# Performance work log

Hardware: AMD Instinct MI355X
Metric: run time of the kernel (lower is better)

The kernel has to match this reference:

```python
import jax, jax.numpy as jnp
import numpy as np


def setup_inputs() -> dict:
    key = jax.random.key(0)
    ks = jax.random.split(key, 4)
    B, S, H = 1, 2048, 2048
    E, I = 32, 768
    scale_h = 1.0 / np.sqrt(H)
    scale_i = 1.0 / np.sqrt(I)
    return {
        "hidden_states": jax.random.normal(ks[0], (B, S, H), dtype=jnp.float32),
        "gate_w": jax.random.normal(ks[1], (E, H), dtype=jnp.float32) * scale_h,
        "gate_up_proj": jax.random.normal(ks[2], (E, H, 2 * I), dtype=jnp.float32) * scale_h,
        "down_proj": jax.random.normal(ks[3], (E, I, H), dtype=jnp.float32) * scale_i,
    }


TOP_K = 4


def reference(hidden_states, gate_w, gate_up_proj, down_proj):
    B, S, H = hidden_states.shape
    x = hidden_states.reshape(-1, H)                      # [T, H]
    T = x.shape[0]

    # Router: softmax -> top-k -> renormalize -> scatter back to dense [T, E]
    router_logits = x @ gate_w.T                          # [T, E]
    probs = jax.nn.softmax(router_logits.astype(jnp.float32), axis=-1)
    top_w, top_idx = jax.lax.top_k(probs, TOP_K)          # [T, K]
    top_w = top_w / jnp.sum(top_w, axis=-1, keepdims=True)
    top_w = top_w.astype(x.dtype)
    router_weights = jnp.zeros_like(router_logits).at[
        jnp.arange(T)[:, None], top_idx
    ].set(top_w)                                          # [T, E]

    # Experts (eval path): every expert processes every token, then weight & sum.
    gate_up = jnp.einsum("th,ehi->eti", x, gate_up_proj)  # [E, T, 2I]
    gate, up = jnp.split(gate_up, 2, axis=-1)
    h = up * jax.nn.silu(gate)                            # [E, T, I]
    expert_out = jnp.einsum("eti,eih->eth", h, down_proj)  # [E, T, H]
    out = jnp.einsum("eth,te->th", expert_out, router_weights)  # [T, H]

    return out.reshape(B, S, H), router_logits
```

## Files before the change

### kernel.cpp

```cpp
#include <hip/hip_runtime.h>
#include <hip/hip_bf16.h>

#define T_TOK 2048
#define H_DIM 2048
#define E_NUM 32
#define I_DIM 768
#define TOPK  4
#define S4    (T_TOK * TOPK)

typedef __attribute__((ext_vector_type(8))) short bf16x8;
typedef __attribute__((ext_vector_type(4))) float f32x4;

__device__ __forceinline__ unsigned pk2(float a, float b) {
    __hip_bfloat16 ha = __float2bfloat16(a);
    __hip_bfloat16 hb = __float2bfloat16(b);
    unsigned short ua = *(unsigned short*)&ha;
    unsigned short ub = *(unsigned short*)&hb;
    return (unsigned)ua | ((unsigned)ub << 16);
}

#define MFMA16(a, b, c) __builtin_amdgcn_mfma_f32_16x16x32_bf16(a, b, c, 0, 0, 0)

__global__ __launch_bounds__(64) void router_kernel(
    const float* __restrict__ x, const float* __restrict__ gate_w,
    float* __restrict__ logits_out, int* __restrict__ cnt,
    int* __restrict__ tok_list, float* __restrict__ tok_w,
    int* __restrict__ tok_slots)
{
    const int t = blockIdx.x;
    const int lane = threadIdx.x;
    __shared__ float xs[H_DIM];
    const float4* __restrict__ xv = (const float4*)(x + (size_t)t * H_DIM);
    float4* xsv = (float4*)xs;
#pragma unroll
    for (int i = 0; i < H_DIM / 4 / 64; ++i) xsv[lane + i * 64] = xv[lane + i * 64];
    __syncthreads();

    const int e = lane & 31;
    const int half = lane >> 5;
    const float4* __restrict__ wv = (const float4*)(gate_w + (size_t)e * H_DIM) + half * (H_DIM / 8);
    const float4* __restrict__ xh = ((const float4*)xs) + half * (H_DIM / 8);
    float acc = 0.f;
#pragma unroll 4
    for (int i = 0; i < H_DIM / 8; ++i) {
        float4 w4 = wv[i], x4 = xh[i];
        acc += w4.x * x4.x + w4.y * x4.y + w4.z * x4.z + w4.w * x4.w;
    }
    acc += __shfl_xor(acc, 32, 64);
    if (lane < 32) logits_out[(size_t)t * E_NUM + e] = acc;

    float v = acc;
    float topv[TOPK]; int topi[TOPK];
#pragma unroll
    for (int r = 0; r < TOPK; ++r) {
        float bv = v; int bi = e;
#pragma unroll
        for (int off = 16; off >= 1; off >>= 1) {
            float ov = __shfl_xor(bv, off, 32);
            int   oi = __shfl_xor(bi, off, 32);
            if (ov > bv || (ov == bv && oi < bi)) { bv = ov; bi = oi; }
        }
        topv[r] = bv; topi[r] = bi;
        if (e == bi) v = -1e30f;
    }
    if (lane == 0) {
        float w[TOPK]; float s = 0.f;
#pragma unroll
        for (int r = 0; r < TOPK; ++r) { w[r] = expf(topv[r] - topv[0]); s += w[r]; }
        float inv = 1.f / s;
#pragma unroll
        for (int r = 0; r < TOPK; ++r) {
            int pos = atomicAdd(&cnt[topi[r]], 1);
            tok_list[topi[r] * T_TOK + pos] = t;
            tok_w  [topi[r] * T_TOK + pos] = w[r] * inv;
            tok_slots[t * TOPK + r] = (topi[r] << 12) | pos;
        }
    }
}

__global__ void scan_kernel(const int* __restrict__ cnt, int* __restrict__ slot_base)
{
    if (threadIdx.x == 0) {
        int s = 0;
        for (int e = 0; e < E_NUM; ++e) { slot_base[e] = s; s += cnt[e]; }
        slot_base[E_NUM] = s;
    }
}

__global__ __launch_bounds__(256) void gather_kernel(
    const float* __restrict__ x, const int* __restrict__ cnt,
    const int* __restrict__ slot_base, const int* __restrict__ tok_list,
    unsigned short* __restrict__ xg_t)
{
    const int e = blockIdx.x;
    const int count = cnt[e];
    const int m0 = blockIdx.y * 8;
    if (m0 >= count) return;
    const int s8   = threadIdx.x >> 5;
    const int kc31 = threadIdx.x & 31;
    const int m = m0 + s8;
    if (m >= count) return;
    const int tok  = tok_list[e * T_TOK + m];
    const int slot = slot_base[e] + m;
    const float* __restrict__ src = x + (size_t)tok * H_DIM;
#pragma unroll
    for (int kcq = 0; kcq < 8; ++kcq) {
        const int kc = kcq * 32 + kc31;
        float4 a = *(const float4*)(src + kc * 8);
        float4 b = *(const float4*)(src + kc * 8 + 4);
        uint4 o;
        o.x = pk2(a.x, a.y); o.y = pk2(a.z, a.w);
        o.z = pk2(b.x, b.y); o.w = pk2(b.z, b.w);
        *(uint4*)(xg_t + ((size_t)kc * S4 + slot) * 8) = o;
    }
}

#define GU_NC (H_DIM / 128)
__global__ __launch_bounds__(512, 4) void gateup_mfma(
    const unsigned short* __restrict__ xg_t, const float* __restrict__ gup_w,
    const int* __restrict__ cnt, const int* __restrict__ slot_base,
    const float* __restrict__ tok_w, unsigned short* __restrict__ h_t)
{
    const int e  = blockIdx.x;
    const int nt = blockIdx.y;
    const int mt = blockIdx.z;
    const int count = cnt[e];
    if (mt * 256 >= count) return;
    const int tid  = threadIdx.x;
    const int lane = tid & 63;
    const int w    = tid >> 6;
    const int base = slot_base[e];
    const int l16  = lane & 15, lg = lane >> 4;

    __shared__ unsigned short Bls[2][2][16 * 32 * 8];
    __shared__ float wls[256];

    if (tid < 256) {
        int m = mt * 256 + tid; if (m >= count) m = count - 1;
        wls[tid] = tok_w[e * T_TOK + m];
    }

    int m0 = mt * 256 + w * 32 + l16;      if (m0 >= count) m0 = count - 1;
    int m1 = mt * 256 + w * 32 + 16 + l16; if (m1 >= count) m1 = count - 1;
    const unsigned short* a0b = xg_t + (size_t)(base + m0) * 8;
    const unsigned short* a1b = xg_t + (size_t)(base + m1) * 8;

    const int bhalf = tid >> 8;
    const int sub   = (tid >> 7) & 1;
    const int t7    = tid & 127;
    const int kb    = (t7 >> 3) * 2;
    const int n4    = (t7 & 7) * 4;
    const int k8    = kb & 7;
    const int kbh   = kb >> 3;
    const float* __restrict__ bbase =
        gup_w + ((size_t)e * H_DIM + kb) * (2 * I_DIM) + (size_t)bhalf * I_DIM + nt * 32 + n4;

    float4 sv0[2], sv1[2];

#define GU_LOAD(C) do { _Pragma("unroll") for (int q2 = 0; q2 < 2; ++q2) { \
        const int q = sub + q2 * 2; \
        const float* s_ = bbase + (size_t)((C) * 128 + q * 32) * (2 * I_DIM); \
        sv0[q2] = *(const float4*)s_; \
        sv1[q2] = *(const float4*)(s_ + 2 * I_DIM); } } while (0)
#define GU_WRITE(BUF) do { _Pragma("unroll") for (int q2 = 0; q2 < 2; ++q2) { \
        const int q = sub + q2 * 2; \
        unsigned short* bw_ = &Bls[BUF][bhalf][((q * 4 + kbh) * 32) * 8]; \
        float p0[4] = {sv0[q2].x, sv0[q2].y, sv0[q2].z, sv0[q2].w}; \
        float p1[4] = {sv1[q2].x, sv1[q2].y, sv1[q2].z, sv1[q2].w}; \
        _Pragma("unroll") for (int j = 0; j < 4; ++j) \
            *(unsigned*)&bw_[(n4 + j) * 8 + k8] = pk2(p0[j], p1[j]); } } while (0)

    f32x4 accg[2][2], accu[2][2];
#pragma unroll
    for (int i = 0; i < 2; ++i)
#pragma unroll
        for (int f = 0; f < 2; ++f) { accg[i][f] = {0.f,0.f,0.f,0.f}; accu[i][f] = {0.f,0.f,0.f,0.f}; }

    GU_LOAD(0);
    GU_WRITE(0);

    for (int c = 0; c < GU_NC; ++c) {
        const int buf = c & 1;
        __syncthreads();
        if (c + 1 < GU_NC) GU_LOAD(c + 1);
#pragma unroll
        for (int s = 0; s < 4; ++s) {
            const size_t aoff = (size_t)(c * 16 + s * 4 + lg) * (S4 * 8);
            bf16x8 a0 = *(const bf16x8*)(a0b + aoff);
            bf16x8 a1 = *(const bf16x8*)(a1b + aoff);
            const unsigned short* bg_ = &Bls[buf][0][((s * 4 + lg) * 32 + l16) * 8];
            const unsigned short* bu_ = &Bls[buf][1][((s * 4 + lg) * 32 + l16) * 8];
            bf16x8 g0 = *(const bf16x8*)(bg_);
            bf16x8 g1 = *(const bf16x8*)(bg_ + 128);
            bf16x8 u0 = *(const bf16x8*)(bu_);
            bf16x8 u1 = *(const bf16x8*)(bu_ + 128);
            accg[0][0] = MFMA16(a0, g0, accg[0][0]);
            accg[0][1] = MFMA16(a0, g1, accg[0][1]);
            accu[0][0] = MFMA16(a0, u0, accu[0][0]);
            accu[0][1] = MFMA16(a0, u1, accu[0][1]);
            accg[1][0] = MFMA16(a1, g0, accg[1][0]);
            accg[1][1] = MFMA16(a1, g1, accg[1][1]);
            accu[1][0] = MFMA16(a1, u0, accu[1][0]);
            accu[1][1] = MFMA16(a1, u1, accu[1][1]);
        }
        if (c + 1 < GU_NC) GU_WRITE((c + 1) & 1);
    }
#undef GU_LOAD
#undef GU_WRITE

#pragma unroll
    for (int i = 0; i < 2; ++i) {
        const int mloc = w * 32 + i * 16 + lg * 4;
#pragma unroll
        for (int r = 0; r < 4; ++r) {
            const int mrow = mt * 256 + mloc + r;
            if (mrow < count) {
                const float wgt = wls[mloc + r];
                const size_t slot = (size_t)(base + mrow);
#pragma unroll
                for (int f = 0; f < 2; ++f) {
                    const int col = nt * 32 + f * 16 + l16;
                    float g = accg[i][f][r], u = accu[i][f][r];
                    float sv = g / (1.f + expf(-g));
                    __hip_bfloat16 hb = __float2bfloat16(wgt * u * sv);
                    h_t[((size_t)(col >> 3) * S4 + slot) * 8 + (col & 7)] = *(unsigned short*)&hb;
                }
            }
        }
    }
}

#define DN_NC (I_DIM / 128)
__global__ __launch_bounds__(512, 4) void down_mfma(
    const unsigned short* __restrict__ h_t, const float* __restrict__ down_w,
    const int* __restrict__ cnt, const int* __restrict__ slot_base,
    float* __restrict__ ods)
{
    const int e  = blockIdx.x;
    const int nt = blockIdx.y;
    const int mt = blockIdx.z;
    const int count = cnt[e];
    if (mt * 256 >= count) return;
    const int tid  = threadIdx.x;
    const int lane = tid & 63;
    const int w    = tid >> 6;
    const int base = slot_base[e];
    const int l16  = lane & 15, lg = lane >> 4;

    __shared__ unsigned short Bls[2][16 * 64 * 8];

    int m0 = mt * 256 + w * 32 + l16;      if (m0 >= count) m0 = count - 1;
    int m1 = mt * 256 + w * 32 + 16 + l16; if (m1 >= count) m1 = count - 1;
    const unsigned short* a0b = h_t + (size_t)(base + m0) * 8;
    const unsigned short* a1b = h_t + (size_t)(base + m1) * 8;

    const int sub = tid >> 8;
    const int t8  = tid & 255;
    const int kb  = (t8 >> 4) * 2;
    const int n4  = (t8 & 15) * 4;
    const int k8  = kb & 7;
    const int kbh = kb >> 3;
    const float* __restrict__ bbase =
        down_w + ((size_t)e * I_DIM + kb) * H_DIM + nt * 64 + n4;

    float4 sv0[2], sv1[2];

#define DN_LOAD(C) do { _Pragma("unroll") for (int q2 = 0; q2 < 2; ++q2) { \
        const int q = sub + q2 * 2; \
        const float* s_ = bbase + (size_t)((C) * 128 + q * 32) * H_DIM; \
        sv0[q2] = *(const float4*)s_; \
        sv1[q2] = *(const float4*)(s_ + H_DIM); } } while (0)
#define DN_WRITE(BUF) do { _Pragma("unroll") for (int q2 = 0; q2 < 2; ++q2) { \
        const int q = sub + q2 * 2; \
        unsigned short* bw_ = &Bls[BUF][((q * 4 + kbh) * 64) * 8]; \
        float p0[4] = {sv0[q2].x, sv0[q2].y, sv0[q2].z, sv0[q2].w}; \
        float p1[4] = {sv1[q2].x, sv1[q2].y, sv1[q2].z, sv1[q2].w}; \
        _Pragma("unroll") for (int j = 0; j < 4; ++j) \
            *(unsigned*)&bw_[(n4 + j) * 8 + k8] = pk2(p0[j], p1[j]); } } while (0)

    f32x4 acc[2][4];
#pragma unroll
    for (int i = 0; i < 2; ++i)
#pragma unroll
        for (int f = 0; f < 4; ++f) acc[i][f] = {0.f,0.f,0.f,0.f};

    DN_LOAD(0);
    DN_WRITE(0);

    for (int c = 0; c < DN_NC; ++c) {
        const int buf = c & 1;
        __syncthreads();
        if (c + 1 < DN_NC) DN_LOAD(c + 1);
#pragma unroll
        for (int s = 0; s < 4; ++s) {
            const size_t aoff = (size_t)(c * 16 + s * 4 + lg) * (S4 * 8);
            bf16x8 a0 = *(const bf16x8*)(a0b + aoff);
            bf16x8 a1 = *(const bf16x8*)(a1b + aoff);
            const unsigned short* bf_ = &Bls[buf][((s * 4 + lg) * 64 + l16) * 8];
            bf16x8 b0 = *(const bf16x8*)(bf_);
            bf16x8 b1 = *(const bf16x8*)(bf_ + 128);
            bf16x8 b2 = *(const bf16x8*)(bf_ + 256);
            bf16x8 b3 = *(const bf16x8*)(bf_ + 384);
            acc[0][0] = MFMA16(a0, b0, acc[0][0]);
            acc[0][1] = MFMA16(a0, b1, acc[0][1]);
            acc[0][2] = MFMA16(a0, b2, acc[0][2]);
            acc[0][3] = MFMA16(a0, b3, acc[0][3]);
            acc[1][0] = MFMA16(a1, b0, acc[1][0]);
            acc[1][1] = MFMA16(a1, b1, acc[1][1]);
            acc[1][2] = MFMA16(a1, b2, acc[1][2]);
            acc[1][3] = MFMA16(a1, b3, acc[1][3]);
        }
        if (c + 1 < DN_NC) DN_WRITE((c + 1) & 1);
    }
#undef DN_LOAD
#undef DN_WRITE

#pragma unroll
    for (int i = 0; i < 2; ++i) {
        const int mloc = w * 32 + i * 16 + lg * 4;
#pragma unroll
        for (int r = 0; r < 4; ++r) {
            const int mrow = mt * 256 + mloc + r;
            if (mrow < count) {
                float* orow = ods + (size_t)(base + mrow) * H_DIM + nt * 64;
#pragma unroll
                for (int f = 0; f < 4; ++f)
                    orow[f * 16 + l16] = acc[i][f][r];
            }
        }
    }
}

__global__ __launch_bounds__(256) void combine_kernel(
    const float* __restrict__ ods, const int* __restrict__ tok_slots,
    const int* __restrict__ slot_base, float* __restrict__ out)
{
    const int t = blockIdx.x;
    const int c0 = threadIdx.x * 8;
    const float* rows[TOPK];
#pragma unroll
    for (int r = 0; r < TOPK; ++r) {
        const int pk = tok_slots[t * TOPK + r];
        const int e = pk >> 12, pos = pk & 4095;
        rows[r] = ods + (size_t)(slot_base[e] + pos) * H_DIM + c0;
    }
    float4 a0 = {0.f,0.f,0.f,0.f}, a1 = {0.f,0.f,0.f,0.f};
#pragma unroll
    for (int r = 0; r < TOPK; ++r) {
        float4 v0 = *(const float4*)(rows[r]);
        float4 v1 = *(const float4*)(rows[r] + 4);
        a0.x += v0.x; a0.y += v0.y; a0.z += v0.z; a0.w += v0.w;
        a1.x += v1.x; a1.y += v1.y; a1.z += v1.z; a1.w += v1.w;
    }
    float* o = out + (size_t)t * H_DIM + c0;
    *(float4*)o = a0;
    *(float4*)(o + 4) = a1;
}

extern "C" void kernel_launch(void* const* d_in, const int* in_sizes, int n_in,
                              void* d_out, int out_size, void* d_ws, size_t ws_size,
                              hipStream_t stream) {
    const float* x      = (const float*)d_in[0];
    const float* gate_w = (const float*)d_in[1];
    const float* gup_w  = (const float*)d_in[2];
    const float* down_w = (const float*)d_in[3];
    float* out    = (float*)d_out;

    char* wsp = (char*)d_ws;
    int*   cnt       = (int*)(wsp);
    int*   slot_base = (int*)(wsp + 256);
    int*   tok_list  = (int*)(wsp + 4096);
    float* tok_w     = (float*)(wsp + 4096 + (size_t)E_NUM * T_TOK * 4);
    int*   tok_slots = (int*)(wsp + (768u << 10));
    unsigned short* xg_t = (unsigned short*)(wsp + (1u << 20));
    unsigned short* h_t  = (unsigned short*)(wsp + (1u << 20) + (size_t)S4 * H_DIM * 2);
    float* ods = (float*)(wsp + (1u << 20) + (size_t)S4 * H_DIM * 2 + (size_t)S4 * I_DIM * 2);

    hipMemsetAsync(cnt, 0, 256, stream);

    router_kernel<<<T_TOK, 64, 0, stream>>>(x, gate_w, out + (size_t)T_TOK * H_DIM,
                                            cnt, tok_list, tok_w, tok_slots);
    scan_kernel<<<1, 64, 0, stream>>>(cnt, slot_base);
    gather_kernel<<<dim3(E_NUM, 256), 256, 0, stream>>>(x, cnt, slot_base, tok_list, xg_t);
    gateup_mfma<<<dim3(E_NUM, 24, 8), 512, 0, stream>>>(
        xg_t, gup_w, cnt, slot_base, tok_w, h_t);
    down_mfma<<<dim3(E_NUM, 32, 8), 512, 0, stream>>>(
        h_t, down_w, cnt, slot_base, ods);
    combine_kernel<<<T_TOK, 256, 0, stream>>>(ods, tok_slots, slot_base, out);
}
```

Baseline: 458.7 us.

## Pre-pack expert weights to bf16 tile images and stage via global_load_lds

Result: slower. 514.5 us (+12.2%).

```diff
diff --git a/kernel.cpp b/kernel.cpp
--- a/kernel.cpp
+++ b/kernel.cpp
@@ -7,6 +7,8 @@
 #define I_DIM 768
 #define TOPK  4
 #define S4    (T_TOK * TOPK)
+#define GU_IMG 8192
+#define DN_IMG 8192
 
 typedef __attribute__((ext_vector_type(8))) short bf16x8;
 typedef __attribute__((ext_vector_type(4))) float f32x4;
@@ -17,6 +19,12 @@
     unsigned short ua = *(unsigned short*)&ha;
     unsigned short ub = *(unsigned short*)&hb;
     return (unsigned)ua | ((unsigned)ub << 16);
+}
+
+__device__ __forceinline__ void gld16(const void* g, void* l) {
+    __builtin_amdgcn_global_load_lds(
+        (const __attribute__((address_space(1))) void*)g,
+        (__attribute__((address_space(3))) void*)l, 16, 0, 0);
 }
 
 #define MFMA16(a, b, c) __builtin_amdgcn_mfma_f32_16x16x32_bf16(a, b, c, 0, 0, 0)
@@ -84,6 +92,70 @@
         int s = 0;
         for (int e = 0; e < E_NUM; ++e) { slot_base[e] = s; s += cnt[e]; }
         slot_base[E_NUM] = s;
+    }
+}
+
+__global__ __launch_bounds__(256) void pack_gu(
+    const float* __restrict__ gup_w, unsigned short* __restrict__ pgu)
+{
+    const int e  = blockIdx.x;
+    const int kg = blockIdx.y;
+    const int c  = kg >> 4, kk = kg & 15;
+    __shared__ unsigned short ls[8][1538];
+    const float* __restrict__ src = gup_w + ((size_t)e * H_DIM + kg * 8) * (2 * I_DIM);
+#pragma unroll
+    for (int r = 0; r < 8; ++r) {
+        const float4* s4 = (const float4*)(src + (size_t)r * (2 * I_DIM));
+        for (int i = threadIdx.x; i < (2 * I_DIM) / 4; i += 256) {
+            float4 v = s4[i];
+            *(unsigned*)&ls[r][i * 4]     = pk2(v.x, v.y);
+            *(unsigned*)&ls[r][i * 4 + 2] = pk2(v.z, v.w);
+        }
+    }
+    __syncthreads();
+    for (int g = threadIdx.x; g < 2 * I_DIM; g += 256) {
+        const int half = g >= I_DIM;
+        const int cg = g - half * I_DIM;
+        const int nt = cg >> 5, n = cg & 31;
+        uint4 o;
+        o.x = (unsigned)ls[0][g] | ((unsigned)ls[1][g] << 16);
+        o.y = (unsigned)ls[2][g] | ((unsigned)ls[3][g] << 16);
+        o.z = (unsigned)ls[4][g] | ((unsigned)ls[5][g] << 16);
+        o.w = (unsigned)ls[6][g] | ((unsigned)ls[7][g] << 16);
+        unsigned short* dst = pgu + ((size_t)(e * 24 + nt) * 16 + c) * GU_IMG
+                            + ((half * 16 + kk) * 32 + n) * 8;
+        *(uint4*)dst = o;
+    }
+}
+
+__global__ __launch_bounds__(256) void pack_dn(
+    const float* __restrict__ down_w, unsigned short* __restrict__ pdn)
+{
+    const int e  = blockIdx.x;
+    const int kg = blockIdx.y;
+    const int c  = kg >> 4, kk = kg & 15;
+    __shared__ unsigned short ls[8][2050];
+    const float* __restrict__ src = down_w + ((size_t)e * I_DIM + kg * 8) * H_DIM;
+#pragma unroll
+    for (int r = 0; r < 8; ++r) {
+        const float4* s4 = (const float4*)(src + (size_t)r * H_DIM);
+        for (int i = threadIdx.x; i < H_DIM / 4; i += 256) {
+            float4 v = s4[i];
+            *(unsigned*)&ls[r][i * 4]     = pk2(v.x, v.y);
+            *(unsigned*)&ls[r][i * 4 + 2] = pk2(v.z, v.w);
+        }
+    }
+    __syncthreads();
+    for (int g = threadIdx.x; g < H_DIM; g += 256) {
+        const int nt = g >> 6, n = g & 63;
+        uint4 o;
+        o.x = (unsigned)ls[0][g] | ((unsigned)ls[1][g] << 16);
+        o.y = (unsigned)ls[2][g] | ((unsigned)ls[3][g] << 16);
+        o.z = (unsigned)ls[4][g] | ((unsigned)ls[5][g] << 16);
+        o.w = (unsigned)ls[6][g] | ((unsigned)ls[7][g] << 16);
+        unsigned short* dst = pdn + ((size_t)(e * 32 + nt) * 6 + c) * DN_IMG
+                            + (kk * 64 + n) * 8;
+        *(uint4*)dst = o;
     }
 }
 
@@ -117,7 +189,7 @@
 
 #define GU_NC (H_DIM / 128)
 __global__ __launch_bounds__(512, 4) void gateup_mfma(
-    const unsigned short* __restrict__ xg_t, const float* __restrict__ gup_w,
+    const unsigned short* __restrict__ xg_t, const unsigned short* __restrict__ pgu,
     const int* __restrict__ cnt, const int* __restrict__ slot_base,
     const float* __restrict__ tok_w, unsigned short* __restrict__ h_t)
 {
@@ -132,7 +204,7 @@
     const int base = slot_base[e];
     const int l16  = lane & 15, lg = lane >> 4;
 
-    __shared__ unsigned short Bls[2][2][16 * 32 * 8];
+    __shared__ unsigned short Bls[2][GU_IMG];
     __shared__ float wls[256];
 
     if (tid < 256) {
@@ -145,30 +217,12 @@
     const unsigned short* a0b = xg_t + (size_t)(base + m0) * 8;
     const unsigned short* a1b = xg_t + (size_t)(base + m1) * 8;
 
-    const int bhalf = tid >> 8;
-    const int sub   = (tid >> 7) & 1;
-    const int t7    = tid & 127;
-    const int kb    = (t7 >> 3) * 2;
-    const int n4    = (t7 & 7) * 4;
-    const int k8    = kb & 7;
-    const int kbh   = kb >> 3;
-    const float* __restrict__ bbase =
-        gup_w + ((size_t)e * H_DIM + kb) * (2 * I_DIM) + (size_t)bhalf * I_DIM + nt * 32 + n4;
-
-    float4 sv0[2], sv1[2];
-
-#define GU_LOAD(C) do { _Pragma("unroll") for (int q2 = 0; q2 < 2; ++q2) { \
-        const int q = sub + q2 * 2; \
-        const float* s_ = bbase + (size_t)((C) * 128 + q * 32) * (2 * I_DIM); \
-        sv0[q2] = *(const float4*)s_; \
-        sv1[q2] = *(const float4*)(s_ + 2 * I_DIM); } } while (0)
-#define GU_WRITE(BUF) do { _Pragma("unroll") for (int q2 = 0; q2 < 2; ++q2) { \
-        const int q = sub + q2 * 2; \
-        unsigned short* bw_ = &Bls[BUF][bhalf][((q * 4 + kbh) * 32) * 8]; \
-        float p0[4] = {sv0[q2].x, sv0[q2].y, sv0[q2].z, sv0[q2].w}; \
-        float p1[4] = {sv1[q2].x, sv1[q2].y, sv1[q2].z, sv1[q2].w}; \
-        _Pragma("unroll") for (int j = 0; j < 4; ++j) \
-            *(unsigned*)&bw_[(n4 + j) * 8 + k8] = pk2(p0[j], p1[j]); } } while (0)
+    const unsigned short* __restrict__ bimg = pgu + ((size_t)(e * 24 + nt) * 16) * GU_IMG;
+
+#define GU_STAGE(C, BUF) do { \
+    const unsigned short* s_ = bimg + (size_t)(C) * GU_IMG + w * 1024 + lane * 8; \
+    gld16(s_,       &Bls[BUF][w * 1024]); \
+    gld16(s_ + 512, &Bls[BUF][w * 1024 + 512]); } while (0)
 
     f32x4 accg[2][2], accu[2][2];
 #pragma unroll
@@ -176,20 +230,19 @@
 #pragma unroll
         for (int f = 0; f < 2; ++f) { accg[i][f] = {0.f,0.f,0.f,0.f}; accu[i][f] = {0.f,0.f,0.f,0.f}; }
 
-    GU_LOAD(0);
-    GU_WRITE(0);
+    GU_STAGE(0, 0);
 
     for (int c = 0; c < GU_NC; ++c) {
         const int buf = c & 1;
         __syncthreads();
-        if (c + 1 < GU_NC) GU_LOAD(c + 1);
+        if (c + 1 < GU_NC) GU_STAGE(c + 1, buf ^ 1);
 #pragma unroll
         for (int s = 0; s < 4; ++s) {
             const size_t aoff = (size_t)(c * 16 + s * 4 + lg) * (S4 * 8);
             bf16x8 a0 = *(const bf16x8*)(a0b + aoff);
             bf16x8 a1 = *(const bf16x8*)(a1b + aoff);
-            const unsigned short* bg_ = &Bls[buf][0][((s * 4 + lg) * 32 + l16) * 8];
-            const unsigned short* bu_ = &Bls[buf][1][((s * 4 + lg) * 32 + l16) * 8];
+            const unsigned short* bg_ = &Bls[buf][((s * 4 + lg) * 32 + l16) * 8];
+            const unsigned short* bu_ = bg_ + 4096;
             bf16x8 g0 = *(const bf16x8*)(bg_);
             bf16x8 g1 = *(const bf16x8*)(bg_ + 128);
             bf16x8 u0 = *(const bf16x8*)(bu_);
@@ -203,10 +256,8 @@
             accu[1][0] = MFMA16(a1, u0, accu[1][0]);
             accu[1][1] = MFMA16(a1, u1, accu[1][1]);
         }
-        if (c + 1 < GU_NC) GU_WRITE((c + 1) & 1);
-    }
-#undef GU_LOAD
-#undef GU_WRITE
+    }
+#undef GU_STAGE
 
 #pragma unroll
     for (int i = 0; i < 2; ++i) {
@@ -232,7 +283,7 @@
 
 #define DN_NC (I_DIM / 128)
 __global__ __launch_bounds__(512, 4) void down_mfma(
-    const unsigned short* __restrict__ h_t, const float* __restrict__ down_w,
+    const unsigned short* __restrict__ h_t, const unsigned short* __restrict__ pdn,
     const int* __restrict__ cnt, const int* __restrict__ slot_base,
     float* __restrict__ ods)
 {
@@ -247,36 +298,19 @@
     const int base = slot_base[e];
     const int l16  = lane & 15, lg = lane >> 4;
 
-    __shared__ unsigned short Bls[2][16 * 64 * 8];
+    __shared__ unsigned short Bls[2][DN_IMG];
 
     int m0 = mt * 256 + w * 32 + l16;      if (m0 >= count) m0 = count - 1;
     int m1 = mt * 256 + w * 32 + 16 + l16; if (m1 >= count) m1 = count - 1;
     const unsigned short* a0b = h_t + (size_t)(base + m0) * 8;
     const unsigned short* a1b = h_t + (size_t)(base + m1) * 8;
 
-    const int sub = tid >> 8;
-    const int t8  = tid & 255;
-    const int kb  = (t8 >> 4) * 2;
-    const int n4  = (t8 & 15) * 4;
-    const int k8  = kb & 7;
-    const int kbh = kb >> 3;
-    const float* __restrict__ bbase =
-        down_w + ((size_t)e * I_DIM + kb) * H_DIM + nt * 64 + n4;
-
-    float4 sv0[2], sv1[2];
-
-#define DN_LOAD(C) do { _Pragma("unroll") for (int q2 = 0; q2 < 2; ++q2) { \
-        const int q = sub + q2 * 2; \
-        const float* s_ = bbase + (size_t)((C) * 128 + q * 32) * H_DIM; \
-        sv0[q2] = *(const float4*)s_; \
-        sv1[q2] = *(const float4*)(s_ + H_DIM); } } while (0)
-#define DN_WRITE(BUF) do { _Pragma("unroll") for (int q2 = 0; q2 < 2; ++q2) { \
-        const int q = sub + q2 * 2; \
-        unsigned short* bw_ = &Bls[BUF][((q * 4 + kbh) * 64) * 8]; \
-        float p0[4] = {sv0[q2].x, sv0[q2].y, sv0[q2].z, sv0[q2].w}; \
-        float p1[4] = {sv1[q2].x, sv1[q2].y, sv1[q2].z, sv1[q2].w}; \
-        _Pragma("unroll") for (int j = 0; j < 4; ++j) \
-            *(unsigned*)&bw_[(n4 + j) * 8 + k8] = pk2(p0[j], p1[j]); } } while (0)
+    const unsigned short* __restrict__ bimg = pdn + ((size_t)(e * 32 + nt) * 6) * DN_IMG;
+
+#define DN_STAGE(C, BUF) do { \
+    const unsigned short* s_ = bimg + (size_t)(C) * DN_IMG + w * 1024 + lane * 8; \
+    gld16(s_,       &Bls[BUF][w * 1024]); \
+    gld16(s_ + 512, &Bls[BUF][w * 1024 + 512]); } while (0)
 
     f32x4 acc[2][4];
 #pragma unroll
@@ -284,13 +318,12 @@
 #pragma unroll
         for (int f = 0; f < 4; ++f) acc[i][f] = {0.f,0.f,0.f,0.f};
 
-    DN_LOAD(0);
-    DN_WRITE(0);
+    DN_STAGE(0, 0);
 
     for (int c = 0; c < DN_NC; ++c) {
         const int buf = c & 1;
         __syncthreads();
-        if (c + 1 < DN_NC) DN_LOAD(c + 1);
+        if (c + 1 < DN_NC) DN_STAGE(c + 1, buf ^ 1);
 #pragma unroll
         for (int s = 0; s < 4; ++s) {
             const size_t aoff = (size_t)(c * 16 + s * 4 + lg) * (S4 * 8);
@@ -310,10 +343,8 @@
             acc[1][2] = MFMA16(a1, b2, acc[1][2]);
             acc[1][3] = MFMA16(a1, b3, acc[1][3]);
         }
-        if (c + 1 < DN_NC) DN_WRITE((c + 1) & 1);
-    }
-#undef DN_LOAD
-#undef DN_WRITE
+    }
+#undef DN_STAGE
 
 #pragma unroll
     for (int i = 0; i < 2; ++i) {
@@ -372,19 +403,25 @@
     int*   tok_list  = (int*)(wsp + 4096);
     float* tok_w     = (float*)(wsp + 4096 + (size_t)E_NUM * T_TOK * 4);
     int*   tok_slots = (int*)(wsp + (768u << 10));
-    unsigned short* xg_t = (unsigned short*)(wsp + (1u << 20));
-    unsigned short* h_t  = (unsigned short*)(wsp + (1u << 20) + (size_t)S4 * H_DIM * 2);
-    float* ods = (float*)(wsp + (1u << 20) + (size_t)S4 * H_DIM * 2 + (size_t)S4 * I_DIM * 2);
+
+    size_t off = (size_t)1 << 20;
+    unsigned short* xg_t = (unsigned short*)(wsp + off); off += (size_t)S4 * H_DIM * 2;
+    unsigned short* h_t  = (unsigned short*)(wsp + off); off += (size_t)S4 * I_DIM * 2;
+    float*          ods  = (float*)(wsp + off);          off += (size_t)S4 * H_DIM * 4;
+    unsigned short* pgu  = (unsigned short*)(wsp + off); off += (size_t)E_NUM * 24 * 16 * GU_IMG * 2;
+    unsigned short* pdn  = (unsigned short*)(wsp + off); off += (size_t)E_NUM * 32 * 6 * DN_IMG * 2;
 
     hipMemsetAsync(cnt, 0, 256, stream);
 
     router_kernel<<<T_TOK, 64, 0, stream>>>(x, gate_w, out + (size_t)T_TOK * H_DIM,
                                             cnt, tok_list, tok_w, tok_slots);
     scan_kernel<<<1, 64, 0, stream>>>(cnt, slot_base);
+    pack_gu<<<dim3(E_NUM, 256), 256, 0, stream>>>(gup_w, pgu);
+    pack_dn<<<dim3(E_NUM, 96), 256, 0, stream>>>(down_w, pdn);
     gather_kernel<<<dim3(E_NUM, 256), 256, 0, stream>>>(x, cnt, slot_base, tok_list, xg_t);
     gateup_mfma<<<dim3(E_NUM, 24, 8), 512, 0, stream>>>(
-        xg_t, gup_w, cnt, slot_base, tok_w, h_t);
+        xg_t, pgu, cnt, slot_base, tok_w, h_t);
     down_mfma<<<dim3(E_NUM, 32, 8), 512, 0, stream>>>(
-        h_t, down_w, cnt, slot_base, ods);
+        h_t, pdn, cnt, slot_base, ods);
     combine_kernel<<<T_TOK, 256, 0, stream>>>(ods, tok_slots, slot_base, out);
 }
```

## Split-K both expert GEMMs with atomic accumulation and separate SiLU pass

Applied to the files above, without the earlier changes.

Result: slower. 666.4 us (+45.3%).

```diff
diff --git a/kernel.cpp b/kernel.cpp
--- a/kernel.cpp
+++ b/kernel.cpp
@@ -20,6 +20,13 @@
 }
 
 #define MFMA16(a, b, c) __builtin_amdgcn_mfma_f32_16x16x32_bf16(a, b, c, 0, 0, 0)
+
+__global__ __launch_bounds__(256) void zero_kernel(uint4* __restrict__ p, long n16)
+{
+    long i = (long)blockIdx.x * 256 + threadIdx.x;
+    long stride = (long)gridDim.x * 256;
+    for (; i < n16; i += stride) p[i] = (uint4){0u, 0u, 0u, 0u};
+}
 
 __global__ __launch_bounds__(64) void router_kernel(
     const float* __restrict__ x, const float* __restrict__ gate_w,
@@ -90,7 +97,8 @@
 __global__ __launch_bounds__(256) void gather_kernel(
     const float* __restrict__ x, const int* __restrict__ cnt,
     const int* __restrict__ slot_base, const int* __restrict__ tok_list,
-    unsigned short* __restrict__ xg_t)
+    const float* __restrict__ tok_w, unsigned short* __restrict__ xg_t,
+    float* __restrict__ slot_w)
 {
     const int e = blockIdx.x;
     const int count = cnt[e];
@@ -102,6 +110,7 @@
     if (m >= count) return;
     const int tok  = tok_list[e * T_TOK + m];
     const int slot = slot_base[e] + m;
+    if (kc31 == 0) slot_w[slot] = tok_w[e * T_TOK + m];
     const float* __restrict__ src = x + (size_t)tok * H_DIM;
 #pragma unroll
     for (int kcq = 0; kcq < 8; ++kcq) {
@@ -115,15 +124,15 @@
     }
 }
 
-#define GU_NC (H_DIM / 128)
-__global__ __launch_bounds__(512, 4) void gateup_mfma(
+__global__ __launch_bounds__(512, 4) void gu_partial(
     const unsigned short* __restrict__ xg_t, const float* __restrict__ gup_w,
     const int* __restrict__ cnt, const int* __restrict__ slot_base,
-    const float* __restrict__ tok_w, unsigned short* __restrict__ h_t)
+    float* __restrict__ gacc, float* __restrict__ uacc)
 {
     const int e  = blockIdx.x;
     const int nt = blockIdx.y;
-    const int mt = blockIdx.z;
+    const int mt = blockIdx.z >> 2;
+    const int ks = blockIdx.z & 3;
     const int count = cnt[e];
     if (mt * 256 >= count) return;
     const int tid  = threadIdx.x;
@@ -133,12 +142,6 @@
     const int l16  = lane & 15, lg = lane >> 4;
 
     __shared__ unsigned short Bls[2][2][16 * 32 * 8];
-    __shared__ float wls[256];
-
-    if (tid < 256) {
-        int m = mt * 256 + tid; if (m >= count) m = count - 1;
-        wls[tid] = tok_w[e * T_TOK + m];
-    }
 
     int m0 = mt * 256 + w * 32 + l16;      if (m0 >= count) m0 = count - 1;
     int m1 = mt * 256 + w * 32 + 16 + l16; if (m1 >= count) m1 = count - 1;
@@ -176,13 +179,15 @@
 #pragma unroll
         for (int f = 0; f < 2; ++f) { accg[i][f] = {0.f,0.f,0.f,0.f}; accu[i][f] = {0.f,0.f,0.f,0.f}; }
 
-    GU_LOAD(0);
+    const int c0 = ks * 4;
+    GU_LOAD(c0);
     GU_WRITE(0);
 
-    for (int c = 0; c < GU_NC; ++c) {
-        const int buf = c & 1;
+    for (int cc = 0; cc < 4; ++cc) {
+        const int c = c0 + cc;
+        const int buf = cc & 1;
         __syncthreads();
-        if (c + 1 < GU_NC) GU_LOAD(c + 1);
+        if (cc + 1 < 4) GU_LOAD(c + 1);
 #pragma unroll
         for (int s = 0; s < 4; ++s) {
             const size_t aoff = (size_t)(c * 16 + s * 4 + lg) * (S4 * 8);
@@ -203,7 +208,7 @@
             accu[1][0] = MFMA16(a1, u0, accu[1][0]);
             accu[1][1] = MFMA16(a1, u1, accu[1][1]);
         }
-        if (c + 1 < GU_NC) GU_WRITE((c + 1) & 1);
+        if (cc + 1 < 4) GU_WRITE(buf ^ 1);
     }
 #undef GU_LOAD
 #undef GU_WRITE
@@ -215,30 +220,53 @@
         for (int r = 0; r < 4; ++r) {
             const int mrow = mt * 256 + mloc + r;
             if (mrow < count) {
-                const float wgt = wls[mloc + r];
                 const size_t slot = (size_t)(base + mrow);
 #pragma unroll
                 for (int f = 0; f < 2; ++f) {
                     const int col = nt * 32 + f * 16 + l16;
-                    float g = accg[i][f][r], u = accu[i][f][r];
-                    float sv = g / (1.f + expf(-g));
-                    __hip_bfloat16 hb = __float2bfloat16(wgt * u * sv);
-                    h_t[((size_t)(col >> 3) * S4 + slot) * 8 + (col & 7)] = *(unsigned short*)&hb;
+                    atomicAdd(&gacc[slot * I_DIM + col], accg[i][f][r]);
+                    atomicAdd(&uacc[slot * I_DIM + col], accu[i][f][r]);
                 }
             }
         }
     }
 }
 
-#define DN_NC (I_DIM / 128)
-__global__ __launch_bounds__(512, 4) void down_mfma(
+__global__ __launch_bounds__(256) void silu_h(
+    const float* __restrict__ gacc, const float* __restrict__ uacc,
+    const float* __restrict__ slot_w, unsigned short* __restrict__ h_t)
+{
+    const int slot = blockIdx.x * 2 + (threadIdx.x >> 7);
+    const int j = threadIdx.x & 127;
+    if (j >= 96) return;
+    const float wgt = slot_w[slot];
+    const float* gp = gacc + (size_t)slot * I_DIM + j * 8;
+    const float* up = uacc + (size_t)slot * I_DIM + j * 8;
+    float4 g0 = *(const float4*)gp, g1 = *(const float4*)(gp + 4);
+    float4 u0 = *(const float4*)up, u1 = *(const float4*)(up + 4);
+    float gv[8] = {g0.x, g0.y, g0.z, g0.w, g1.x, g1.y, g1.z, g1.w};
+    float uv[8] = {u0.x, u0.y, u0.z, u0.w, u1.x, u1.y, u1.z, u1.w};
+    float hv[8];
+#pragma unroll
+    for (int k = 0; k < 8; ++k) {
+        float g = gv[k];
+        hv[k] = wgt * uv[k] * (g / (1.f + expf(-g)));
+    }
+    uint4 o;
+    o.x = pk2(hv[0], hv[1]); o.y = pk2(hv[2], hv[3]);
+    o.z = pk2(hv[4], hv[5]); o.w = pk2(hv[6], hv[7]);
+    *(uint4*)(h_t + ((size_t)j * S4 + slot) * 8) = o;
+}
+
+__global__ __launch_bounds__(512, 4) void dn_partial(
     const unsigned short* __restrict__ h_t, const float* __restrict__ down_w,
     const int* __restrict__ cnt, const int* __restrict__ slot_base,
     float* __restrict__ ods)
 {
     const int e  = blockIdx.x;
     const int nt = blockIdx.y;
-    const int mt = blockIdx.z;
+    const int mt = blockIdx.z / 3;
+    const int ks = blockIdx.z % 3;
     const int count = cnt[e];
     if (mt * 256 >= count) return;
     const int tid  = threadIdx.x;
@@ -284,13 +312,15 @@
 #pragma unroll
         for (int f = 0; f < 4; ++f) acc[i][f] = {0.f,0.f,0.f,0.f};
 
-    DN_LOAD(0);
+    const int c0 = ks * 2;
+    DN_LOAD(c0);
     DN_WRITE(0);
 
-    for (int c = 0; c < DN_NC; ++c) {
-        const int buf = c & 1;
+    for (int cc = 0; cc < 2; ++cc) {
+        const int c = c0 + cc;
+        const int buf = cc & 1;
         __syncthreads();
-        if (c + 1 < DN_NC) DN_LOAD(c + 1);
+        if (cc + 1 < 2) DN_LOAD(c + 1);
 #pragma unroll
         for (int s = 0; s < 4; ++s) {
             const size_t aoff = (size_t)(c * 16 + s * 4 + lg) * (S4 * 8);
@@ -310,7 +340,7 @@
             acc[1][2] = MFMA16(a1, b2, acc[1][2]);
             acc[1][3] = MFMA16(a1, b3, acc[1][3]);
         }
-        if (c + 1 < DN_NC) DN_WRITE((c + 1) & 1);
+        if (cc + 1 < 2) DN_WRITE(buf ^ 1);
     }
 #undef DN_LOAD
 #undef DN_WRITE
@@ -325,7 +355,7 @@
                 float* orow = ods + (size_t)(base + mrow) * H_DIM + nt * 64;
 #pragma unroll
                 for (int f = 0; f < 4; ++f)
-                    orow[f * 16 + l16] = acc[i][f][r];
+                    atomicAdd(&orow[f * 16 + l16], acc[i][f][r]);
             }
         }
     }
@@ -372,19 +402,28 @@
     int*   tok_list  = (int*)(wsp + 4096);
     float* tok_w     = (float*)(wsp + 4096 + (size_t)E_NUM * T_TOK * 4);
     int*   tok_slots = (int*)(wsp + (768u << 10));
-    unsigned short* xg_t = (unsigned short*)(wsp + (1u << 20));
-    unsigned short* h_t  = (unsigned short*)(wsp + (1u << 20) + (size_t)S4 * H_DIM * 2);
-    float* ods = (float*)(wsp + (1u << 20) + (size_t)S4 * H_DIM * 2 + (size_t)S4 * I_DIM * 2);
+    float* slot_w    = (float*)(wsp + (832u << 10));
+
+    size_t off = (size_t)1 << 20;
+    unsigned short* xg_t = (unsigned short*)(wsp + off); off += (size_t)S4 * H_DIM * 2;
+    unsigned short* h_t  = (unsigned short*)(wsp + off); off += (size_t)S4 * I_DIM * 2;
+    float* gacc = (float*)(wsp + off);
+    float* uacc = gacc + (size_t)S4 * I_DIM;
+    float* ods  = uacc + (size_t)S4 * I_DIM;
+    const long zero16 = ((size_t)S4 * I_DIM * 2 + (size_t)S4 * H_DIM) / 4;
 
     hipMemsetAsync(cnt, 0, 256, stream);
+    zero_kernel<<<4096, 256, 0, stream>>>((uint4*)gacc, zero16);
 
     router_kernel<<<T_TOK, 64, 0, stream>>>(x, gate_w, out + (size_t)T_TOK * H_DIM,
                                             cnt, tok_list, tok_w, tok_slots);
     scan_kernel<<<1, 64, 0, stream>>>(cnt, slot_base);
-    gather_kernel<<<dim3(E_NUM, 256), 256, 0, stream>>>(x, cnt, slot_base, tok_list, xg_t);
-    gateup_mfma<<<dim3(E_NUM, 24, 8), 512, 0, stream>>>(
-        xg_t, gup_w, cnt, slot_base, tok_w, h_t);
-    down_mfma<<<dim3(E_NUM, 32, 8), 512, 0, stream>>>(
+    gather_kernel<<<dim3(E_NUM, 256), 256, 0, stream>>>(x, cnt, slot_base, tok_list,
+                                                        tok_w, xg_t, slot_w);
+    gu_partial<<<dim3(E_NUM, 24, 32), 512, 0, stream>>>(
+        xg_t, gup_w, cnt, slot_base, gacc, uacc);
+    silu_h<<<S4 / 2, 256, 0, stream>>>(gacc, uacc, slot_w, h_t);
+    dn_partial<<<dim3(E_NUM, 32, 24), 512, 0, stream>>>(
         h_t, down_w, cnt, slot_base, ods);
     combine_kernel<<<T_TOK, 256, 0, stream>>>(ods, tok_slots, slot_base, out);
 }
```
